# Kernel optimization log

Measured on AMD Instinct MI355X. Metric: run time of the kernel, lower is better.

Reference implementation:

```python
import jax, jax.numpy as jnp
import numpy as np

B, S, D = 2, 2048, 1024
N_HEADS = 16
HEAD_DIM = D // N_HEADS
D_FF = 4 * D
EPS = 1e-5


def setup_inputs() -> dict:
    key = jax.random.key(0)
    ks = jax.random.split(key, 16)
    s = 0.02
    return {
        "x": jax.random.normal(ks[0], (B, S, D), dtype=jnp.float32),
        "ln1_scale": jnp.ones((D,), jnp.float32),
        "ln1_shift": jnp.zeros((D,), jnp.float32),
        "wq": jax.random.normal(ks[1], (D, D), jnp.float32) * s,
        "wk": jax.random.normal(ks[2], (D, D), jnp.float32) * s,
        "wv": jax.random.normal(ks[3], (D, D), jnp.float32) * s,
        "wo": jax.random.normal(ks[4], (D, D), jnp.float32) * s,
        "bo": jnp.zeros((D,), jnp.float32),
        "ln2_scale": jnp.ones((D,), jnp.float32),
        "ln2_shift": jnp.zeros((D,), jnp.float32),
        "w1": jax.random.normal(ks[5], (D, D_FF), jnp.float32) * s,
        "b1": jnp.zeros((D_FF,), jnp.float32),
        "w2": jax.random.normal(ks[6], (D_FF, D), jnp.float32) * s,
        "b2": jnp.zeros((D,), jnp.float32),
    }


def _layer_norm(x, scale, shift):
    mean = jnp.mean(x, axis=-1, keepdims=True)
    var = jnp.var(x, axis=-1, keepdims=True)  # unbiased=False
    return (x - mean) / jnp.sqrt(var + EPS) * scale + shift


def _mha(x, wq, wk, wv, wo, bo):
    b, s, d = x.shape
    q = (x @ wq).reshape(b, s, N_HEADS, HEAD_DIM).transpose(0, 2, 1, 3)
    k = (x @ wk).reshape(b, s, N_HEADS, HEAD_DIM).transpose(0, 2, 1, 3)
    v = (x @ wv).reshape(b, s, N_HEADS, HEAD_DIM).transpose(0, 2, 1, 3)
    scores = jnp.einsum('bhqd,bhkd->bhqk', q, k)
    causal = jnp.tril(jnp.ones((s, s), dtype=bool))  # mask upper triangle
    scores = jnp.where(causal, scores, -jnp.inf)
    attn = jax.nn.softmax(scores / np.sqrt(HEAD_DIM).astype(np.float32), axis=-1)
    ctx = jnp.einsum('bhqk,bhkd->bhqd', attn, v)
    ctx = ctx.transpose(0, 2, 1, 3).reshape(b, s, d)
    return ctx @ wo + bo


def reference(x, ln1_scale, ln1_shift, wq, wk, wv, wo, bo,
              ln2_scale, ln2_shift, w1, b1, w2, b2):
    # Attention sub-block (dropout is identity in eval / droprate=0)
    h = x + _mha(_layer_norm(x, ln1_scale, ln1_shift), wq, wk, wv, wo, bo)
    # FFN sub-block (note: original code discards the dropout(inp) result and
    # returns shortcut + ff_output, which is the standard residual)
    y = _layer_norm(h, ln2_scale, ln2_shift)
    ff = jax.nn.gelu(y @ w1 + b1, approximate=True) @ w2 + b2
    return h + ff
```

## Files before the change

### kernel.cpp

```cpp
#include <hip/hip_runtime.h>
#include <hip/hip_bf16.h>

typedef unsigned short u16;
typedef unsigned int u32;
typedef __bf16 bf16x8 __attribute__((ext_vector_type(8)));
typedef float f32x4 __attribute__((ext_vector_type(4)));

#if __has_builtin(__builtin_amdgcn_exp2f)
#define FEXP2 __builtin_amdgcn_exp2f
#else
#define FEXP2 exp2f
#endif

#define QSCALE 0.1803368801f

__device__ __forceinline__ u16 f2bf(float f) {
  __hip_bfloat16 h = __float2bfloat16(f);
  return __builtin_bit_cast(u16, h);
}

__device__ __forceinline__ void load_lds16(const u16* g, u16* l) {
  __builtin_amdgcn_global_load_lds((const __attribute__((address_space(1))) void*)g,
                                   (__attribute__((address_space(3))) void*)l, 16, 0, 0);
}

__global__ __launch_bounds__(256) void tconv_kernel(const float* __restrict__ src,
                                                    u16* __restrict__ dst, int R, int C) {
  __shared__ float tile[32][33];
  int bx = blockIdx.x * 32, by = blockIdx.y * 32;
  int tx = threadIdx.x, ty = threadIdx.y;
#pragma unroll
  for (int i = 0; i < 4; ++i)
    tile[ty + 8 * i][tx] = src[(size_t)(by + ty + 8 * i) * C + bx + tx];
  __syncthreads();
#pragma unroll
  for (int i = 0; i < 4; ++i)
    dst[(size_t)(bx + ty + 8 * i) * R + by + tx] = f2bf(tile[tx][ty + 8 * i]);
}

__global__ __launch_bounds__(256) void ln_kernel(const float* __restrict__ src,
                                                 u16* __restrict__ dst,
                                                 const float* __restrict__ gamma,
                                                 const float* __restrict__ beta) {
  int row = blockIdx.x, tid = threadIdx.x;
  const float4 v = ((const float4*)(src + (size_t)row * 1024))[tid];
  float s = v.x + v.y + v.z + v.w;
  float q = v.x * v.x + v.y * v.y + v.z * v.z + v.w * v.w;
#pragma unroll
  for (int off = 32; off >= 1; off >>= 1) {
    s += __shfl_down(s, off, 64);
    q += __shfl_down(q, off, 64);
  }
  __shared__ float red[8];
  if ((tid & 63) == 0) { red[(tid >> 6) * 2] = s; red[(tid >> 6) * 2 + 1] = q; }
  __syncthreads();
  s = red[0] + red[2] + red[4] + red[6];
  q = red[1] + red[3] + red[5] + red[7];
  float mean = s * (1.0f / 1024.0f);
  float var = q * (1.0f / 1024.0f) - mean * mean;
  float rstd = rsqrtf(var + 1e-5f);
  float4 g = ((const float4*)gamma)[tid];
  float4 b = ((const float4*)beta)[tid];
  ushort4 o;
  o.x = f2bf((v.x - mean) * rstd * g.x + b.x);
  o.y = f2bf((v.y - mean) * rstd * g.y + b.y);
  o.z = f2bf((v.z - mean) * rstd * g.z + b.z);
  o.w = f2bf((v.w - mean) * rstd * g.w + b.w);
  *(ushort4*)(dst + (size_t)row * 1024 + tid * 4) = o;
}

template <int MODE, int BN>
__global__ __launch_bounds__(256) void gemm_st(const u16* __restrict__ A,
                                               const u16* __restrict__ BT,
                                               int M, int N, int K,
                                               const float* __restrict__ bias,
                                               const float* __restrict__ resid,
                                               void* __restrict__ outp,
                                               void* __restrict__ outp2,
                                               void* __restrict__ outp3) {
  constexpr int NJ = BN / 32;
  const int tid = threadIdx.x, lane = tid & 63, wave = tid >> 6;
  const int l16 = lane & 15, quad = lane >> 4;
  const int mblk = blockIdx.y * 128, nblk = blockIdx.x * BN;
  const int m0w = (wave >> 1) * 64, n0w = (wave & 1) * (BN / 2);

  __shared__ u16 Ab[128 * 32];
  __shared__ u16 Bb[BN * 32];

  f32x4 acc[4][NJ];
#pragma unroll
  for (int i = 0; i < 4; ++i)
#pragma unroll
    for (int j = 0; j < NJ; ++j)
#pragma unroll
      for (int r = 0; r < 4; ++r) acc[i][j][r] = 0.0f;

  const int srow = lane >> 2, schunk = lane & 3;
  const u16* gA = A + (size_t)(mblk + wave * 32 + srow) * K + schunk * 8;
  u16* lA = Ab + (wave * 32) * 32;
  const u16* gB;
  u16* lB;
  if constexpr (BN == 128) {
    gB = BT + (size_t)(nblk + wave * 32 + srow) * K + schunk * 8;
    lB = Bb + (wave * 32) * 32;
  } else {
    gB = BT + (size_t)(nblk + wave * 16 + srow) * K + schunk * 8;
    lB = Bb + (wave * 16) * 32;
  }

  for (int k0 = 0; k0 < K; k0 += 32) {
    __syncthreads();
    load_lds16(gA + k0, lA);
    load_lds16(gA + 16 * (size_t)K + k0, lA + 16 * 32);
    if constexpr (BN == 128) {
      load_lds16(gB + k0, lB);
      load_lds16(gB + 16 * (size_t)K + k0, lB + 16 * 32);
    } else {
      load_lds16(gB + k0, lB);
    }
    asm volatile("s_waitcnt vmcnt(0)" ::: "memory");
    __syncthreads();

    bf16x8 af[4], bfr[NJ];
#pragma unroll
    for (int i = 0; i < 4; ++i)
      af[i] = *(const bf16x8*)(Ab + (m0w + i * 16 + l16) * 32 + quad * 8);
#pragma unroll
    for (int j = 0; j < NJ; ++j)
      bfr[j] = *(const bf16x8*)(Bb + (n0w + j * 16 + l16) * 32 + quad * 8);
#pragma unroll
    for (int i = 0; i < 4; ++i)
#pragma unroll
      for (int j = 0; j < NJ; ++j)
        acc[i][j] = __builtin_amdgcn_mfma_f32_16x16x32_bf16(af[i], bfr[j], acc[i][j], 0, 0, 0);
  }

#pragma unroll
  for (int i = 0; i < 4; ++i) {
#pragma unroll
    for (int j = 0; j < NJ; ++j) {
      const int col = nblk + n0w + j * 16 + l16;
#pragma unroll
      for (int r = 0; r < 4; ++r) {
        const int row = mblk + m0w + i * 16 + quad * 4 + r;
        float v = acc[i][j][r];
        if constexpr (MODE == 0) {
          const int slotc = col >> 6;
          const int ty = slotc >> 4;
          const int h = slotc & 15, d = col & 63;
          const int bb = row >> 11, s = row & 2047;
          if (ty == 0) {
            ((u16*)outp)[(((size_t)(bb * 16 + h)) * 2048 + s) * 64 + d] = f2bf(v * QSCALE);
          } else if (ty == 1) {
            ((u16*)outp2)[(((size_t)(bb * 16 + h)) * 2048 + s) * 64 + d] = f2bf(v);
          } else {
            const int spos = (s & ~31) | ((s & 15) << 1) | ((s >> 4) & 1);
            ((u16*)outp3)[(((size_t)(bb * 16 + h)) * 64 + d) * 2048 + spos] = f2bf(v);
          }
        } else if constexpr (MODE == 3) {
          ((float*)outp)[(size_t)row * N + col] = v + bias[col] + resid[(size_t)row * N + col];
        } else if constexpr (MODE == 4) {
          float u = v + bias[col];
          float c = 0.7978845608f * u * (1.0f + 0.044715f * u * u);
          float a = fabsf(c);
          float e = __expf(-2.0f * a);
          float th = (1.0f - e) / (1.0f + e);
          th = copysignf(th, c);
          ((u16*)outp)[(size_t)row * N + col] = f2bf(0.5f * u * (1.0f + th));
        } else if constexpr (MODE == 5) {
          ((float*)outp)[(size_t)row * N + col] =
              v + bias[col] + resid[(size_t)row * N + col];
        }
      }
    }
  }
}

__global__ __launch_bounds__(128) void attn_kernel(const u16* __restrict__ Q,
                                                   const u16* __restrict__ Kb,
                                                   const u16* __restrict__ VT,
                                                   u16* __restrict__ ctx) {
  const int tid = threadIdx.x, lane = tid & 63, wave = tid >> 6;
  const int l16 = lane & 15, quad = lane >> 4;
  const int id = blockIdx.x, xcd = id & 7, slot = id >> 3;
  const int bh = xcd + 8 * (slot & 3);
  const int qt = 31 - (slot >> 2);
  const int b = bh >> 4, hh = bh & 15;
  const int q0 = qt * 64 + wave * 32;

  const u16* qp = Q + (size_t)bh * 2048 * 64;
  const u16* kp = Kb + (size_t)bh * 2048 * 64;
  const u16* vp = VT + (size_t)bh * 64 * 2048;

  bf16x8 qf[2][2];
#pragma unroll
  for (int rf = 0; rf < 2; ++rf)
#pragma unroll
    for (int kk = 0; kk < 2; ++kk)
      qf[rf][kk] = *(const bf16x8*)(qp + (size_t)(q0 + rf * 16 + l16) * 64 + kk * 32 + quad * 8);

  f32x4 o[2][4], lac[2];
#pragma unroll
  for (int rf = 0; rf < 2; ++rf) {
#pragma unroll
    for (int r = 0; r < 4; ++r) lac[rf][r] = 0.0f;
#pragma unroll
    for (int dt = 0; dt < 4; ++dt)
#pragma unroll
      for (int r = 0; r < 4; ++r) o[rf][dt][r] = 0.0f;
  }

  bf16x8 onef;
#pragma unroll
  for (int i = 0; i < 8; ++i) onef[i] = (__bf16)1.0f;

  __shared__ u16 pbuf[2][32 * 40];
  u16* pw = pbuf[wave];

  const int nfull = q0 >> 5;

  bf16x8 kf[2][2], vf[4], kfn[2][2], vfn[4];
#pragma unroll
  for (int st = 0; st < 2; ++st)
#pragma unroll
    for (int kk = 0; kk < 2; ++kk)
      kf[st][kk] = *(const bf16x8*)(kp + (size_t)(st * 16 + l16) * 64 + kk * 32 + quad * 8);
#pragma unroll
  for (int dt = 0; dt < 4; ++dt)
    vf[dt] = *(const bf16x8*)(vp + (size_t)(dt * 16 + l16) * 2048 + quad * 8);

  for (int kt = 0; kt <= nfull; ++kt) {
    const int kb0 = kt * 32;
    f32x4 sc[2][2];
#pragma unroll
    for (int rf = 0; rf < 2; ++rf)
#pragma unroll
      for (int st = 0; st < 2; ++st) {
#pragma unroll
        for (int r = 0; r < 4; ++r) sc[rf][st][r] = 0.0f;
#pragma unroll
        for (int kk = 0; kk < 2; ++kk)
          sc[rf][st] = __builtin_amdgcn_mfma_f32_16x16x32_bf16(qf[rf][kk], kf[st][kk], sc[rf][st], 0, 0, 0);
      }

    const int kbn = (kt < nfull) ? kb0 + 32 : 0;
#pragma unroll
    for (int st = 0; st < 2; ++st)
#pragma unroll
      for (int kk = 0; kk < 2; ++kk)
        kfn[st][kk] = *(const bf16x8*)(kp + (size_t)(kbn + st * 16 + l16) * 64 + kk * 32 + quad * 8);
#pragma unroll
    for (int dt = 0; dt < 4; ++dt)
      vfn[dt] = *(const bf16x8*)(vp + (size_t)(dt * 16 + l16) * 2048 + kbn + quad * 8);

    const bool masked = (kt == nfull);
#pragma unroll
    for (int rf = 0; rf < 2; ++rf)
#pragma unroll
      for (int r = 0; r < 4; ++r) {
        float s0 = sc[rf][0][r], s1 = sc[rf][1][r];
        if (masked) {
          const int rel = rf * 16 + quad * 4 + r;
          if (l16 > rel) s0 = -INFINITY;
          if (16 + l16 > rel) s1 = -INFINITY;
        }
        const u32 pk = (u32)f2bf(FEXP2(s0)) | ((u32)f2bf(FEXP2(s1)) << 16);
        *(u32*)(pw + (rf * 16 + quad * 4 + r) * 40 + l16 * 2) = pk;
      }
    asm volatile("s_waitcnt lgkmcnt(0)" ::: "memory");
#pragma unroll
    for (int rf = 0; rf < 2; ++rf) {
      bf16x8 pf = *(const bf16x8*)(pw + (rf * 16 + l16) * 40 + quad * 8);
      lac[rf] = __builtin_amdgcn_mfma_f32_16x16x32_bf16(pf, onef, lac[rf], 0, 0, 0);
#pragma unroll
      for (int dt = 0; dt < 4; ++dt)
        o[rf][dt] = __builtin_amdgcn_mfma_f32_16x16x32_bf16(pf, vf[dt], o[rf][dt], 0, 0, 0);
    }
#pragma unroll
    for (int st = 0; st < 2; ++st)
#pragma unroll
      for (int kk = 0; kk < 2; ++kk) kf[st][kk] = kfn[st][kk];
#pragma unroll
    for (int dt = 0; dt < 4; ++dt) vf[dt] = vfn[dt];
  }

#pragma unroll
  for (int rf = 0; rf < 2; ++rf)
#pragma unroll
    for (int r = 0; r < 4; ++r) {
      const float inv = 1.0f / lac[rf][r];
      const int row = q0 + rf * 16 + quad * 4 + r;
#pragma unroll
      for (int dt = 0; dt < 4; ++dt) {
        const int col = dt * 16 + l16;
        ctx[((size_t)(b * 2048 + row)) * 1024 + hh * 64 + col] = f2bf(o[rf][dt][r] * inv);
      }
    }
}

extern "C" void kernel_launch(void* const* d_in, const int* in_sizes, int n_in,
                              void* d_out, int out_size, void* d_ws, size_t ws_size,
                              hipStream_t stream) {
  (void)in_sizes; (void)n_in; (void)out_size; (void)ws_size;
  const float* x    = (const float*)d_in[0];
  const float* g1   = (const float*)d_in[1];
  const float* s1   = (const float*)d_in[2];
  const float* wq   = (const float*)d_in[3];
  const float* wk   = (const float*)d_in[4];
  const float* wv   = (const float*)d_in[5];
  const float* wo   = (const float*)d_in[6];
  const float* bo   = (const float*)d_in[7];
  const float* g2   = (const float*)d_in[8];
  const float* s2   = (const float*)d_in[9];
  const float* w1   = (const float*)d_in[10];
  const float* b1   = (const float*)d_in[11];
  const float* w2   = (const float*)d_in[12];
  const float* b2   = (const float*)d_in[13];

  char* ws = (char*)d_ws;
  u16* wqkvT = (u16*)(ws + 0);
  u16* woT   = (u16*)(ws + 6291456);
  u16* w1T   = (u16*)(ws + 8388608);
  u16* w2T   = (u16*)(ws + 16777216);
  u16* xn    = (u16*)(ws + 25165824);
  u16* qb    = (u16*)(ws + 33554432);
  u16* kb    = (u16*)(ws + 41943040);
  u16* vT    = (u16*)(ws + 50331648);
  u16* ctx   = (u16*)(ws + 58720256);
  u16* f     = (u16*)(ws + 33554432);
  float* h   = (float*)(ws + 67108864);
  u16* y     = xn;

  dim3 tb(32, 8);
  tconv_kernel<<<dim3(32, 32), tb, 0, stream>>>(wq, wqkvT, 1024, 1024);
  tconv_kernel<<<dim3(32, 32), tb, 0, stream>>>(wk, wqkvT + 1024 * 1024, 1024, 1024);
  tconv_kernel<<<dim3(32, 32), tb, 0, stream>>>(wv, wqkvT + 2048 * 1024, 1024, 1024);
  tconv_kernel<<<dim3(32, 32), tb, 0, stream>>>(wo, woT, 1024, 1024);
  tconv_kernel<<<dim3(128, 32), tb, 0, stream>>>(w1, w1T, 1024, 4096);
  tconv_kernel<<<dim3(32, 128), tb, 0, stream>>>(w2, w2T, 4096, 1024);

  ln_kernel<<<4096, 256, 0, stream>>>(x, xn, g1, s1);

  gemm_st<0, 128><<<dim3(24, 32), 256, 0, stream>>>(xn, wqkvT, 4096, 3072, 1024,
                                                    nullptr, nullptr, qb, kb, vT);

  attn_kernel<<<1024, 128, 0, stream>>>(qb, kb, vT, ctx);

  gemm_st<3, 64><<<dim3(16, 32), 256, 0, stream>>>(ctx, woT, 4096, 1024, 1024, bo, x, h,
                                                   nullptr, nullptr);

  ln_kernel<<<4096, 256, 0, stream>>>(h, y, g2, s2);

  gemm_st<4, 128><<<dim3(32, 32), 256, 0, stream>>>(y, w1T, 4096, 4096, 1024, b1, nullptr, f,
                                                    nullptr, nullptr);
  gemm_st<5, 64><<<dim3(16, 32), 256, 0, stream>>>(f, w2T, 4096, 1024, 4096, b2, h, (float*)d_out,
                                                   nullptr, nullptr);
}
```

Before: 425.6 us.

## Deepen GEMM K-step, remap blocks per XCD, pair attention tiles, cheaper GELU

GEMM kernels now load two 32-wide K slices per barrier pair (K step of 64), halving synchronisation count, and blocks are remapped so each XCD works on a contiguous band of rows for L2 reuse. Attention blocks now hold four waves that pair a late (long) query tile with an early (short) one to balance causal work, and the P packing uses a manual bit-twiddled bf16 pack. The GELU epilogue is rewritten as u*sigmoid form using exp2 and a hardware reciprocal. Risks include higher LDS use, launch_bounds occupancy hint changes, and slight numeric differences from the approximate reciprocal.

```diff
diff --git a/kernel.cpp b/kernel.cpp
--- a/kernel.cpp
+++ b/kernel.cpp
@@ -12,11 +12,25 @@
 #define FEXP2 exp2f
 #endif
 
+#if __has_builtin(__builtin_amdgcn_rcpf)
+#define FRCP __builtin_amdgcn_rcpf
+#else
+#define FRCP(x) (1.0f / (x))
+#endif
+
 #define QSCALE 0.1803368801f
 
 __device__ __forceinline__ u16 f2bf(float f) {
   __hip_bfloat16 h = __float2bfloat16(f);
   return __builtin_bit_cast(u16, h);
+}
+
+__device__ __forceinline__ u32 pack2_bf16(float a, float b) {
+  u32 ua = __builtin_bit_cast(u32, a);
+  ua += 0x7FFFu + ((ua >> 16) & 1u);
+  u32 ub = __builtin_bit_cast(u32, b);
+  ub += 0x7FFFu + ((ub >> 16) & 1u);
+  return (ua >> 16) | (ub & 0xFFFF0000u);
 }
 
 __device__ __forceinline__ void load_lds16(const u16* g, u16* l) {
@@ -69,23 +83,57 @@
   *(ushort4*)(dst + (size_t)row * 1024 + tid * 4) = o;
 }
 
+template <int MODE>
+__device__ __forceinline__ void epilogue_elem(float v, int row, int col, int N,
+                                              const float* __restrict__ bias,
+                                              const float* __restrict__ resid,
+                                              void* __restrict__ outp,
+                                              void* __restrict__ outp2,
+                                              void* __restrict__ outp3) {
+  if constexpr (MODE == 0) {
+    const int slotc = col >> 6;
+    const int ty = slotc >> 4;
+    const int h = slotc & 15, d = col & 63;
+    const int bb = row >> 11, s = row & 2047;
+    if (ty == 0) {
+      ((u16*)outp)[(((size_t)(bb * 16 + h)) * 2048 + s) * 64 + d] = f2bf(v * QSCALE);
+    } else if (ty == 1) {
+      ((u16*)outp2)[(((size_t)(bb * 16 + h)) * 2048 + s) * 64 + d] = f2bf(v);
+    } else {
+      const int spos = (s & ~31) | ((s & 15) << 1) | ((s >> 4) & 1);
+      ((u16*)outp3)[(((size_t)(bb * 16 + h)) * 64 + d) * 2048 + spos] = f2bf(v);
+    }
+  } else if constexpr (MODE == 3) {
+    ((float*)outp)[(size_t)row * N + col] = v + bias[col] + resid[(size_t)row * N + col];
+  } else if constexpr (MODE == 4) {
+    float u = v + bias[col];
+    float c = u * (0.7978845608f + 0.0356774081f * u * u);
+    float t = FEXP2(c * -2.885390082f);
+    ((u16*)outp)[(size_t)row * N + col] = f2bf(u * FRCP(1.0f + t));
+  } else if constexpr (MODE == 5) {
+    ((float*)outp)[(size_t)row * N + col] = v + bias[col] + resid[(size_t)row * N + col];
+  }
+}
+
 template <int MODE, int BN>
-__global__ __launch_bounds__(256) void gemm_st(const u16* __restrict__ A,
-                                               const u16* __restrict__ BT,
-                                               int M, int N, int K,
-                                               const float* __restrict__ bias,
-                                               const float* __restrict__ resid,
-                                               void* __restrict__ outp,
-                                               void* __restrict__ outp2,
-                                               void* __restrict__ outp3) {
+__global__ __launch_bounds__(256, 2) void gemm2(const u16* __restrict__ A,
+                                                const u16* __restrict__ BT,
+                                                int M, int N, int K, int nbx,
+                                                const float* __restrict__ bias,
+                                                const float* __restrict__ resid,
+                                                void* __restrict__ outp,
+                                                void* __restrict__ outp2,
+                                                void* __restrict__ outp3) {
   constexpr int NJ = BN / 32;
   const int tid = threadIdx.x, lane = tid & 63, wave = tid >> 6;
   const int l16 = lane & 15, quad = lane >> 4;
-  const int mblk = blockIdx.y * 128, nblk = blockIdx.x * BN;
+  const int id = blockIdx.x, xcd = id & 7, s = id >> 3;
+  const int by = xcd * 4 + s / nbx, bx = s - (s / nbx) * nbx;
+  const int mblk = by * 128, nblk = bx * BN;
   const int m0w = (wave >> 1) * 64, n0w = (wave & 1) * (BN / 2);
 
-  __shared__ u16 Ab[128 * 32];
-  __shared__ u16 Bb[BN * 32];
+  __shared__ u16 Ab[2][128 * 32];
+  __shared__ u16 Bb[2][BN * 32];
 
   f32x4 acc[4][NJ];
 #pragma unroll
@@ -97,86 +145,61 @@
 
   const int srow = lane >> 2, schunk = lane & 3;
   const u16* gA = A + (size_t)(mblk + wave * 32 + srow) * K + schunk * 8;
-  u16* lA = Ab + (wave * 32) * 32;
-  const u16* gB;
-  u16* lB;
-  if constexpr (BN == 128) {
-    gB = BT + (size_t)(nblk + wave * 32 + srow) * K + schunk * 8;
-    lB = Bb + (wave * 32) * 32;
-  } else {
-    gB = BT + (size_t)(nblk + wave * 16 + srow) * K + schunk * 8;
-    lB = Bb + (wave * 16) * 32;
-  }
-
-  for (int k0 = 0; k0 < K; k0 += 32) {
+  u16* lA0 = Ab[0] + (wave * 32) * 32;
+  u16* lA1 = Ab[1] + (wave * 32) * 32;
+  const int bwrows = (BN == 128) ? wave * 32 : wave * 16;
+  const u16* gB = BT + (size_t)(nblk + bwrows + srow) * K + schunk * 8;
+  u16* lB0 = Bb[0] + bwrows * 32;
+  u16* lB1 = Bb[1] + bwrows * 32;
+
+  for (int k0 = 0; k0 < K; k0 += 64) {
     __syncthreads();
-    load_lds16(gA + k0, lA);
-    load_lds16(gA + 16 * (size_t)K + k0, lA + 16 * 32);
+    load_lds16(gA + k0, lA0);
+    load_lds16(gA + 16 * (size_t)K + k0, lA0 + 16 * 32);
+    load_lds16(gA + k0 + 32, lA1);
+    load_lds16(gA + 16 * (size_t)K + k0 + 32, lA1 + 16 * 32);
     if constexpr (BN == 128) {
-      load_lds16(gB + k0, lB);
-      load_lds16(gB + 16 * (size_t)K + k0, lB + 16 * 32);
+      load_lds16(gB + k0, lB0);
+      load_lds16(gB + 16 * (size_t)K + k0, lB0 + 16 * 32);
+      load_lds16(gB + k0 + 32, lB1);
+      load_lds16(gB + 16 * (size_t)K + k0 + 32, lB1 + 16 * 32);
     } else {
-      load_lds16(gB + k0, lB);
+      load_lds16(gB + k0, lB0);
+      load_lds16(gB + k0 + 32, lB1);
     }
     asm volatile("s_waitcnt vmcnt(0)" ::: "memory");
     __syncthreads();
 
-    bf16x8 af[4], bfr[NJ];
-#pragma unroll
-    for (int i = 0; i < 4; ++i)
-      af[i] = *(const bf16x8*)(Ab + (m0w + i * 16 + l16) * 32 + quad * 8);
-#pragma unroll
-    for (int j = 0; j < NJ; ++j)
-      bfr[j] = *(const bf16x8*)(Bb + (n0w + j * 16 + l16) * 32 + quad * 8);
-#pragma unroll
-    for (int i = 0; i < 4; ++i)
+#pragma unroll
+    for (int h = 0; h < 2; ++h) {
+      bf16x8 af[4], bfr[NJ];
+#pragma unroll
+      for (int i = 0; i < 4; ++i)
+        af[i] = *(const bf16x8*)(Ab[h] + (m0w + i * 16 + l16) * 32 + quad * 8);
 #pragma unroll
       for (int j = 0; j < NJ; ++j)
-        acc[i][j] = __builtin_amdgcn_mfma_f32_16x16x32_bf16(af[i], bfr[j], acc[i][j], 0, 0, 0);
-  }
-
-#pragma unroll
-  for (int i = 0; i < 4; ++i) {
+        bfr[j] = *(const bf16x8*)(Bb[h] + (n0w + j * 16 + l16) * 32 + quad * 8);
+#pragma unroll
+      for (int i = 0; i < 4; ++i)
+#pragma unroll
+        for (int j = 0; j < NJ; ++j)
+          acc[i][j] = __builtin_amdgcn_mfma_f32_16x16x32_bf16(af[i], bfr[j], acc[i][j], 0, 0, 0);
+    }
+  }
+
+#pragma unroll
+  for (int i = 0; i < 4; ++i)
 #pragma unroll
     for (int j = 0; j < NJ; ++j) {
       const int col = nblk + n0w + j * 16 + l16;
 #pragma unroll
-      for (int r = 0; r < 4; ++r) {
-        const int row = mblk + m0w + i * 16 + quad * 4 + r;
-        float v = acc[i][j][r];
-        if constexpr (MODE == 0) {
-          const int slotc = col >> 6;
-          const int ty = slotc >> 4;
-          const int h = slotc & 15, d = col & 63;
-          const int bb = row >> 11, s = row & 2047;
-          if (ty == 0) {
-            ((u16*)outp)[(((size_t)(bb * 16 + h)) * 2048 + s) * 64 + d] = f2bf(v * QSCALE);
-          } else if (ty == 1) {
-            ((u16*)outp2)[(((size_t)(bb * 16 + h)) * 2048 + s) * 64 + d] = f2bf(v);
-          } else {
-            const int spos = (s & ~31) | ((s & 15) << 1) | ((s >> 4) & 1);
-            ((u16*)outp3)[(((size_t)(bb * 16 + h)) * 64 + d) * 2048 + spos] = f2bf(v);
-          }
-        } else if constexpr (MODE == 3) {
-          ((float*)outp)[(size_t)row * N + col] = v + bias[col] + resid[(size_t)row * N + col];
-        } else if constexpr (MODE == 4) {
-          float u = v + bias[col];
-          float c = 0.7978845608f * u * (1.0f + 0.044715f * u * u);
-          float a = fabsf(c);
-          float e = __expf(-2.0f * a);
-          float th = (1.0f - e) / (1.0f + e);
-          th = copysignf(th, c);
-          ((u16*)outp)[(size_t)row * N + col] = f2bf(0.5f * u * (1.0f + th));
-        } else if constexpr (MODE == 5) {
-          ((float*)outp)[(size_t)row * N + col] =
-              v + bias[col] + resid[(size_t)row * N + col];
-        }
-      }
-    }
-  }
-}
-
-__global__ __launch_bounds__(128) void attn_kernel(const u16* __restrict__ Q,
+      for (int r = 0; r < 4; ++r)
+        epilogue_elem<MODE>(acc[i][j][r], mblk + m0w + i * 16 + quad * 4 + r, col, N,
+                            bias, resid, outp, outp2, outp3);
+    }
+}
+
+__global__ __launch_bounds__(256) void attn_kernel(const u16* __restrict__ Q,
                                                    const u16* __restrict__ Kb,
                                                    const u16* __restrict__ VT,
                                                    u16* __restrict__ ctx) {
@@ -184,9 +207,10 @@
   const int l16 = lane & 15, quad = lane >> 4;
   const int id = blockIdx.x, xcd = id & 7, slot = id >> 3;
   const int bh = xcd + 8 * (slot & 3);
-  const int qt = 31 - (slot >> 2);
+  const int pr = slot >> 2;
+  const int qt = (wave < 2) ? (31 - pr) : pr;
   const int b = bh >> 4, hh = bh & 15;
-  const int q0 = qt * 64 + wave * 32;
+  const int q0 = qt * 64 + (wave & 1) * 32;
 
   const u16* qp = Q + (size_t)bh * 2048 * 64;
   const u16* kp = Kb + (size_t)bh * 2048 * 64;
@@ -214,7 +238,7 @@
 #pragma unroll
   for (int i = 0; i < 8; ++i) onef[i] = (__bf16)1.0f;
 
-  __shared__ u16 pbuf[2][32 * 40];
+  __shared__ u16 pbuf[4][32 * 40];
   u16* pw = pbuf[wave];
 
   const int nfull = q0 >> 5;
@@ -264,8 +288,8 @@
           if (l16 > rel) s0 = -INFINITY;
           if (16 + l16 > rel) s1 = -INFINITY;
         }
-        const u32 pk = (u32)f2bf(FEXP2(s0)) | ((u32)f2bf(FEXP2(s1)) << 16);
-        *(u32*)(pw + (rf * 16 + quad * 4 + r) * 40 + l16 * 2) = pk;
+        *(u32*)(pw + (rf * 16 + quad * 4 + r) * 40 + l16 * 2) =
+            pack2_bf16(FEXP2(s0), FEXP2(s1));
       }
     asm volatile("s_waitcnt lgkmcnt(0)" ::: "memory");
 #pragma unroll
@@ -341,18 +365,18 @@
 
   ln_kernel<<<4096, 256, 0, stream>>>(x, xn, g1, s1);
 
-  gemm_st<0, 128><<<dim3(24, 32), 256, 0, stream>>>(xn, wqkvT, 4096, 3072, 1024,
-                                                    nullptr, nullptr, qb, kb, vT);
-
-  attn_kernel<<<1024, 128, 0, stream>>>(qb, kb, vT, ctx);
-
-  gemm_st<3, 64><<<dim3(16, 32), 256, 0, stream>>>(ctx, woT, 4096, 1024, 1024, bo, x, h,
-                                                   nullptr, nullptr);
+  gemm2<0, 128><<<768, 256, 0, stream>>>(xn, wqkvT, 4096, 3072, 1024, 24,
+                                         nullptr, nullptr, qb, kb, vT);
+
+  attn_kernel<<<512, 256, 0, stream>>>(qb, kb, vT, ctx);
+
+  gemm2<3, 64><<<512, 256, 0, stream>>>(ctx, woT, 4096, 1024, 1024, 16, bo, x, h,
+                                        nullptr, nullptr);
 
   ln_kernel<<<4096, 256, 0, stream>>>(h, y, g2, s2);
 
-  gemm_st<4, 128><<<dim3(32, 32), 256, 0, stream>>>(y, w1T, 4096, 4096, 1024, b1, nullptr, f,
-                                                    nullptr, nullptr);
-  gemm_st<5, 64><<<dim3(16, 32), 256, 0, stream>>>(f, w2T, 4096, 1024, 4096, b2, h, (float*)d_out,
-                                                   nullptr, nullptr);
-}
+  gemm2<4, 128><<<1024, 256, 0, stream>>>(y, w1T, 4096, 4096, 1024, 32,
+                                          b1, nullptr, f, nullptr, nullptr);
+  gemm2<5, 64><<<512, 256, 0, stream>>>(f, w2T, 4096, 1024, 4096, 16, b2, h,
+                                        (float*)d_out, nullptr, nullptr);
+}
```

Result: faster. 365.8 us (-14.0%).
